# Optimization experiments

Measured on AMD Instinct MI355X. Metric: run time of the kernel, lower is better.

## Reference

```python
import jax, jax.numpy as jnp
import numpy as np

NUM_NODES = 50000
NUM_EDGES = 800000
NUM_GRAPHS = 64
EMBED = 128
HIDDEN = 128
LAYERS = 3
CLUSTERS = 16
OUT_DIM = 128
MAX_DEG = 64
EPS = 1e-5


def setup_inputs() -> dict:
    key = jax.random.key(0)
    ks = jax.random.split(key, 16)
    deg_idx = jax.random.randint(ks[0], (NUM_NODES,), 0, MAX_DEG + 1)
    edge_index = jax.random.randint(ks[1], (2, NUM_EDGES), 0, NUM_NODES)
    batch = jnp.sort(jax.random.randint(ks[2], (NUM_NODES,), 0, NUM_GRAPHS))
    s = 0.05
    emb = jax.random.normal(ks[3], (MAX_DEG + 1, EMBED), jnp.float32) * s
    Wl = jax.random.normal(ks[4], (LAYERS, HIDDEN, HIDDEN), jnp.float32) * s
    bl = jnp.zeros((LAYERS, HIDDEN), jnp.float32)
    Wr = jax.random.normal(ks[5], (LAYERS, HIDDEN, HIDDEN), jnp.float32) * s
    gamma = jnp.ones((LAYERS, HIDDEN), jnp.float32)
    beta = jnp.zeros((LAYERS, HIDDEN), jnp.float32)
    attn_W = jax.random.normal(ks[6], (HIDDEN, CLUSTERS), jnp.float32) * s
    attn_b = jnp.zeros((CLUSTERS,), jnp.float32)
    out_W = jax.random.normal(ks[7], (HIDDEN, OUT_DIM), jnp.float32) * s
    out_b = jnp.zeros((OUT_DIM,), jnp.float32)
    return {"emb": emb, "Wl": Wl, "bl": bl, "Wr": Wr, "gamma": gamma,
            "beta": beta, "attn_W": attn_W, "attn_b": attn_b,
            "out_W": out_W, "out_b": out_b, "deg_idx": deg_idx,
            "edge_index": edge_index, "batch": batch}


def reference(emb, Wl, bl, Wr, gamma, beta, attn_W, attn_b, out_W, out_b,
              deg_idx, edge_index, batch):
    N = deg_idx.shape[0]
    src, dst = edge_index[0], edge_index[1]
    x = emb[deg_idx]  # [N, EMBED]
    for l in range(Wl.shape[0]):
        # SAGEConv (mean aggr): lin_l(mean_j x_j) + lin_r(x); lin_r has no bias
        msg_sum = jax.ops.segment_sum(x[src], dst, num_segments=N)
        cnt = jax.ops.segment_sum(jnp.ones((src.shape[0], 1), x.dtype), dst,
                                  num_segments=N)
        mean = msg_sum / jnp.maximum(cnt, 1.0)
        x = mean @ Wl[l] + bl[l] + x @ Wr[l]
        # BatchNorm1d (training-mode batch stats, biased variance)
        mu = x.mean(axis=0)
        var = jnp.mean((x - mu) ** 2, axis=0)
        x = (x - mu) * jax.lax.rsqrt(var + EPS) * gamma[l] + beta[l]
        x = jax.nn.relu(x)  # dropout is identity in eval
    scores = x @ attn_W + attn_b  # [N, C] (num_heads == 1 -> squeeze)
    # per-graph softmax over nodes (segment softmax along dim 0)
    smax = jax.ops.segment_max(scores, batch, num_segments=NUM_GRAPHS)
    e = jnp.exp(scores - smax[batch])
    denom = jax.ops.segment_sum(e, batch, num_segments=NUM_GRAPHS)
    w = e / denom[batch]  # [N, C]
    # c_b = w_b^T @ x_b  -> segment-weighted sums: [B, C, H]
    clust = jax.ops.segment_sum(w[:, :, None] * x[:, None, :], batch,
                                num_segments=NUM_GRAPHS)
    return clust @ out_W + out_b  # [B, C, OUT_DIM]
```

## Files before the change

### kernel.cpp

```cpp
#include <hip/hip_runtime.h>

typedef unsigned short u16;
typedef unsigned int   u32;

#define H    128
#define C    16
#define ODIM 128

typedef short bf16x8 __attribute__((ext_vector_type(8)));
typedef float f32x4  __attribute__((ext_vector_type(4)));
typedef float f32x2v __attribute__((ext_vector_type(2)));

#define WSP 272
#define NP  256

__device__ __forceinline__ float bf2f(u32 v){
  union { u32 i; float f; } t; t.i = v << 16; return t.f;
}
__device__ __forceinline__ u16 f2bf(float f){
  u32 u = __float_as_uint(f);
  u32 r = u + 0x7fffu + ((u >> 16) & 1u);
  return (u16)(r >> 16);
}
__device__ __forceinline__ u32 pack2(float a, float b){
  return (u32)f2bf(a) | ((u32)f2bf(b) << 16);
}
__device__ __forceinline__ u32 pack_fp8x4(float a, float b, float c, float d){
  int p = __builtin_amdgcn_cvt_pk_fp8_f32(a, b, 0, false);
  p     = __builtin_amdgcn_cvt_pk_fp8_f32(c, d, p, true);
  return (u32)p;
}

__global__ __launch_bounds__(256) void k_setup(const float* __restrict__ emb,
    const int* __restrict__ deg, u16* __restrict__ xb, u32* __restrict__ xq,
    const int* __restrict__ batch, int* __restrict__ gs,
    const float* __restrict__ Wl, const float* __restrict__ Wr,
    u16* __restrict__ Wt, const int* __restrict__ ei,
    int* __restrict__ blkhist, int N, int B, int NB, int E, int chunk,
    int g0, int g1, int g2){
  __shared__ __align__(16) char smem[4608];
  int bid = blockIdx.x, tid = threadIdx.x;
  if (bid < g0){
    int i = bid*256 + tid;
    if (i < N*32){
      int n = i >> 5, q = i & 31;
      int d = deg[n];
      float4 v = ((const float4*)(emb + (size_t)d*H))[q];
      uint2 o; o.x = pack2(v.x, v.y); o.y = pack2(v.z, v.w);
      ((uint2*)(xb + (size_t)n*H))[q] = o;
      xq[i] = pack_fp8x4(v.x, v.y, v.z, v.w);
    }
  } else if (bid < g1){
    int n = (bid - g0)*256 + tid;
    if (n < N){
      int b = batch[n];
      if (n == 0){ for (int g = 0; g <= b; g++) gs[g] = 0; }
      else {
        int pb = batch[n-1];
        for (int g = pb+1; g <= b; g++) gs[g] = n;
      }
      if (n == N-1){ for (int g = b+1; g <= B; g++) gs[g] = N; }
    }
  } else if (bid < g2){
    u16 (*T)[18] = (u16(*)[18])smem;
    int b = bid - g1;
    int strip = b & 7, half = (b >> 3) & 1, l = b >> 4;
    const float* M = (half ? Wr : Wl) + (size_t)l*H*H;
    int k0 = strip * 16;
    #pragma unroll
    for (int j = 0; j < 8; j++){
      int u = tid + j*256;
      int kk = u >> 7, h = u & 127;
      T[h][kk] = f2bf(M[(size_t)(k0 + kk)*H + h]);
    }
    __syncthreads();
    #pragma unroll
    for (int j = 0; j < 8; j++){
      int u = tid + j*256;
      int h = u >> 4, k16 = u & 15;
      Wt[((size_t)(l*H + h))*256 + half*128 + k0 + k16] = T[h][k16];
    }
  } else {
    int* hist = (int*)smem;
    int blk = bid - g2;
    for (int b = tid; b < NB; b += 256) hist[b] = 0;
    __syncthreads();
    int start = blk*chunk, end = min(E, start + chunk);
    for (int e = start + tid; e < end; e += 256)
      atomicAdd(&hist[ei[E + e] >> 7], 1);
    __syncthreads();
    for (int b = tid; b < NB; b += 256) blkhist[b*NP + blk] = hist[b];
  }
}

__global__ __launch_bounds__(256) void k_scanA(const int* __restrict__ in,
    int* __restrict__ out, int* __restrict__ bsum, int n){
  __shared__ int wsum[4];
  int tid = threadIdx.x;
  int base = blockIdx.x*1024 + tid*4;
  int v0 = (base+0 < n) ? in[base+0] : 0;
  int v1 = (base+1 < n) ? in[base+1] : 0;
  int v2 = (base+2 < n) ? in[base+2] : 0;
  int v3 = (base+3 < n) ? in[base+3] : 0;
  int tsum = v0+v1+v2+v3;
  int lane = tid & 63, w = tid >> 6;
  int incl = tsum;
  for (int d = 1; d < 64; d <<= 1){
    int t = __shfl_up(incl, d, 64);
    if (lane >= d) incl += t;
  }
  if (lane == 63) wsum[w] = incl;
  __syncthreads();
  int woff = 0;
  for (int i = 0; i < w; i++) woff += wsum[i];
  int excl = woff + incl - tsum;
  if (base+0 < n) out[base+0] = excl;
  if (base+1 < n) out[base+1] = excl + v0;
  if (base+2 < n) out[base+2] = excl + v0 + v1;
  if (base+3 < n) out[base+3] = excl + v0 + v1 + v2;
  if (tid == 255) bsum[blockIdx.x] = woff + incl;
}

__global__ __launch_bounds__(256) void k_scanB(const int* __restrict__ bsum,
    int* __restrict__ boff, int nb){
  __shared__ int ws[4];
  int tid = threadIdx.x;
  int v = (tid < nb) ? bsum[tid] : 0;
  int lane = tid & 63, w = tid >> 6;
  int incl = v;
  for (int d = 1; d < 64; d <<= 1){
    int t = __shfl_up(incl, d, 64);
    if (lane >= d) incl += t;
  }
  if (lane == 63) ws[w] = incl;
  __syncthreads();
  int woff = 0;
  for (int i = 0; i < w; i++) woff += ws[i];
  boff[tid] = woff + incl - v;
}

__global__ __launch_bounds__(256) void k_scanC(int* __restrict__ out,
    const int* __restrict__ boff, int n){
  int i = blockIdx.x*256 + threadIdx.x;
  if (i < n) out[i] += boff[i >> 10];
}

__global__ __launch_bounds__(256) void k_place(const int* __restrict__ ei,
    const int* __restrict__ bases, int2* __restrict__ pairs,
    int NB, int E, int chunk){
  __shared__ int cursor[400];
  int blk = blockIdx.x, tid = threadIdx.x;
  for (int b = tid; b < NB; b += 256) cursor[b] = bases[b*NP + blk];
  __syncthreads();
  int start = blk*chunk, end = min(E, start + chunk);
  for (int e = start + tid; e < end; e += 256){
    int s = ei[e], d = ei[E + e];
    int pos = atomicAdd(&cursor[d >> 7], 1);
    pairs[pos] = make_int2(s, d);
  }
}

__global__ __launch_bounds__(256) void k_cnt_place(const int2* __restrict__ pairs,
    const int* __restrict__ bases, int* __restrict__ rowptr,
    int* __restrict__ col, int NB, int N, int E){
  int b = blockIdx.x, tid = threadIdx.x;
  int bstart = bases[b*NP];
  int bend   = (b+1 < NB) ? bases[(b+1)*NP] : E;
  __shared__ int cnt[128], sc[128], rank[128];
  if (tid < 128) cnt[tid] = 0;
  __syncthreads();
  for (int e = bstart + tid; e < bend; e += 256)
    atomicAdd(&cnt[pairs[e].y & 127], 1);
  __syncthreads();
  if (tid < 128) sc[tid] = cnt[tid];
  for (int d = 1; d < 128; d <<= 1){
    int v = 0;
    __syncthreads();
    if (tid < 128 && tid >= d) v = sc[tid - d];
    __syncthreads();
    if (tid < 128) sc[tid] += v;
  }
  __syncthreads();
  if (tid < 128){
    int excl = sc[tid] - cnt[tid];
    rank[tid] = bstart + excl;
    int node = b*128 + tid;
    if (node < N) rowptr[node] = bstart + excl;
  }
  if (b == NB-1 && tid == 0) rowptr[N] = E;
  __syncthreads();
  for (int e = bstart + tid; e < bend; e += 256){
    int2 p = pairs[e];
    int pos = atomicAdd(&rank[p.y & 127], 1);
    col[pos] = p.x;
  }
}

__global__ __launch_bounds__(256) void k_agg(const u32* __restrict__ xq,
    const int* __restrict__ rowptr, const int* __restrict__ col,
    u16* __restrict__ meanb, int N){
  int wid  = (blockIdx.x*256 + threadIdx.x) >> 6;
  int lane = threadIdx.x & 63;
  if (wid >= N) return;
  int r0 = rowptr[wid], r1 = rowptr[wid+1];
  int grp = lane >> 4, fl = lane & 15;
  const u32* xf = xq + fl*2;
  float a0=0.f,a1=0.f,a2=0.f,a3=0.f,a4=0.f,a5=0.f,a6=0.f,a7=0.f;
  int e = r0 + grp;
  for (; e + 4 < r1; e += 8){
    uint2 v = *(const uint2*)(xf + (size_t)col[e]*32);
    uint2 u = *(const uint2*)(xf + (size_t)col[e+4]*32);
    f32x2v p0 = __builtin_amdgcn_cvt_pk_f32_fp8((int)v.x, false);
    f32x2v p1 = __builtin_amdgcn_cvt_pk_f32_fp8((int)v.x, true);
    f32x2v p2 = __builtin_amdgcn_cvt_pk_f32_fp8((int)v.y, false);
    f32x2v p3 = __builtin_amdgcn_cvt_pk_f32_fp8((int)v.y, true);
    f32x2v q0 = __builtin_amdgcn_cvt_pk_f32_fp8((int)u.x, false);
    f32x2v q1 = __builtin_amdgcn_cvt_pk_f32_fp8((int)u.x, true);
    f32x2v q2 = __builtin_amdgcn_cvt_pk_f32_fp8((int)u.y, false);
    f32x2v q3 = __builtin_amdgcn_cvt_pk_f32_fp8((int)u.y, true);
    a0 += p0.x + q0.x; a1 += p0.y + q0.y;
    a2 += p1.x + q1.x; a3 += p1.y + q1.y;
    a4 += p2.x + q2.x; a5 += p2.y + q2.y;
    a6 += p3.x + q3.x; a7 += p3.y + q3.y;
  }
  if (e < r1){
    uint2 v = *(const uint2*)(xf + (size_t)col[e]*32);
    f32x2v p0 = __builtin_amdgcn_cvt_pk_f32_fp8((int)v.x, false);
    f32x2v p1 = __builtin_amdgcn_cvt_pk_f32_fp8((int)v.x, true);
    f32x2v p2 = __builtin_amdgcn_cvt_pk_f32_fp8((int)v.y, false);
    f32x2v p3 = __builtin_amdgcn_cvt_pk_f32_fp8((int)v.y, true);
    a0 += p0.x; a1 += p0.y; a2 += p1.x; a3 += p1.y;
    a4 += p2.x; a5 += p2.y; a6 += p3.x; a7 += p3.y;
  }
  a0 += __shfl_xor(a0,16,64); a1 += __shfl_xor(a1,16,64);
  a2 += __shfl_xor(a2,16,64); a3 += __shfl_xor(a3,16,64);
  a4 += __shfl_xor(a4,16,64); a5 += __shfl_xor(a5,16,64);
  a6 += __shfl_xor(a6,16,64); a7 += __shfl_xor(a7,16,64);
  a0 += __shfl_xor(a0,32,64); a1 += __shfl_xor(a1,32,64);
  a2 += __shfl_xor(a2,32,64); a3 += __shfl_xor(a3,32,64);
  a4 += __shfl_xor(a4,32,64); a5 += __shfl_xor(a5,32,64);
  a6 += __shfl_xor(a6,32,64); a7 += __shfl_xor(a7,32,64);
  if (grp == 0){
    float invc = 1.0f / (float)max(r1 - r0, 1);
    uint4 o;
    o.x = pack2(a0*invc, a1*invc);
    o.y = pack2(a2*invc, a3*invc);
    o.z = pack2(a4*invc, a5*invc);
    o.w = pack2(a6*invc, a7*invc);
    *(uint4*)(meanb + (size_t)wid*H + fl*8) = o;
  }
}

__global__ __launch_bounds__(256) void k_linear(const u16* __restrict__ meanb,
    const u16* __restrict__ xb, const u16* __restrict__ Wt,
    const float* __restrict__ bl, float* __restrict__ x2,
    float* __restrict__ pstats, int N){
  __shared__ u16 Ws[128][WSP];
  __shared__ float Sh[128], Qh[128];
  int tid = threadIdx.x;
  if (tid < 128){ Sh[tid] = 0.f; Qh[tid] = 0.f; }
  int lane = tid & 63, w = tid >> 6;
  int mlane = lane & 15, quad = lane >> 4;
  int node = blockIdx.x*64 + w*16 + mlane;
  const u16* arow_m = meanb + (size_t)node*H + quad*8;
  const u16* arow_x = xb   + (size_t)node*H + quad*8;
  bf16x8 af[8];
  #pragma unroll
  for (int kk = 0; kk < 4; kk++){
    af[kk]     = *(const bf16x8*)(arow_m + kk*32);
    af[kk + 4] = *(const bf16x8*)(arow_x + kk*32);
  }
  #pragma unroll
  for (int j = 0; j < 16; j++){
    int u = tid + j*256;
    int row = u >> 5, seg = u & 31;
    uint4 v = ((const uint4*)(Wt + (size_t)row*256))[seg];
    *(uint4*)&Ws[row][seg*8] = v;
  }
  __syncthreads();
  f32x4 acc[8];
  #pragma unroll
  for (int t = 0; t < 8; t++) acc[t] = (f32x4){0.f, 0.f, 0.f, 0.f};
  #pragma unroll
  for (int kk = 0; kk < 8; kk++){
    #pragma unroll
    for (int t = 0; t < 8; t++){
      bf16x8 b = *(const bf16x8*)&Ws[t*16 + mlane][kk*32 + quad*8];
      acc[t] = __builtin_amdgcn_mfma_f32_16x16x32_bf16(af[kk], b, acc[t], 0, 0, 0);
    }
  }
  #pragma unroll
  for (int t = 0; t < 8; t++){
    int h = t*16 + mlane;
    float bv = bl[h];
    float s = 0.f, q = 0.f;
    #pragma unroll
    for (int r = 0; r < 4; r++){
      int nd = blockIdx.x*64 + w*16 + quad*4 + r;
      if (nd < N){
        float v = acc[t][r] + bv;
        x2[(size_t)nd*H + h] = v;
        s += v; q = fmaf(v, v, q);
      }
    }
    s += __shfl_xor(s, 16, 64); s += __shfl_xor(s, 32, 64);
    q += __shfl_xor(q, 16, 64); q += __shfl_xor(q, 32, 64);
    if (quad == 0){
      atomicAdd(&Sh[h], s);
      atomicAdd(&Qh[h], q);
    }
  }
  __syncthreads();
  {
    float v = (tid < 128) ? Sh[tid] : Qh[tid - 128];
    pstats[(size_t)blockIdx.x*256 + tid] = v;
  }
}

__global__ __launch_bounds__(256) void k_statred(const float* __restrict__ pstats,
    float* __restrict__ stats, int nblk){
  __shared__ float red[4];
  int c = blockIdx.x, tid = threadIdx.x;
  float s = 0.f;
  for (int b = tid; b < nblk; b += 256)
    s += pstats[(size_t)b*256 + c];
  s += __shfl_xor(s, 1, 64);  s += __shfl_xor(s, 2, 64);
  s += __shfl_xor(s, 4, 64);  s += __shfl_xor(s, 8, 64);
  s += __shfl_xor(s, 16, 64); s += __shfl_xor(s, 32, 64);
  if ((tid & 63) == 0) red[tid >> 6] = s;
  __syncthreads();
  if (tid == 0) stats[c] = red[0] + red[1] + red[2] + red[3];
}

__global__ __launch_bounds__(256) void k_bnrelu(const float* __restrict__ x2,
    const float* __restrict__ stats, const float* __restrict__ gamma,
    const float* __restrict__ beta, u16* __restrict__ xb, u32* __restrict__ xq,
    int N, float invN,
    const float* __restrict__ attn_W, const float* __restrict__ attn_b,
    float* __restrict__ escore, int do_scores){
  __shared__ float xs[8][132];
  __shared__ float aw[H*C];
  __shared__ float ab[C];
  int tid = threadIdx.x;
  int i = blockIdx.x*256 + tid;
  bool active = (i < N*32);
  int h = (tid & 31) * 4;
  float r[4] = {0.f, 0.f, 0.f, 0.f};
  if (active){
    float4 v = ((const float4*)x2)[i];
    float vv[4] = {v.x, v.y, v.z, v.w};
    #pragma unroll
    for (int j = 0; j < 4; j++){
      float mu  = stats[h+j] * invN;
      float var = fmaf(-mu, mu, stats[H + h + j] * invN);
      float sc  = rsqrtf(var + 1e-5f) * gamma[h+j];
      float bi  = beta[h+j];
      r[j] = fmaxf(fmaf(vv[j] - mu, sc, bi), 0.0f);
    }
    uint2 o; o.x = pack2(r[0], r[1]); o.y = pack2(r[2], r[3]);
    ((uint2*)xb)[i] = o;
    xq[i] = pack_fp8x4(r[0], r[1], r[2], r[3]);
  }
  if (do_scores){
    #pragma unroll
    for (int j = 0; j < 8; j++) aw[tid + j*256] = attn_W[tid + j*256];
    if (tid < C) ab[tid] = attn_b[tid];
    int ln = tid >> 5;
    if (active){
      xs[ln][h+0]=r[0]; xs[ln][h+1]=r[1]; xs[ln][h+2]=r[2]; xs[ln][h+3]=r[3];
    }
    __syncthreads();
    if (tid < 128){
      int n2 = tid >> 4, c = tid & 15;
      int node = blockIdx.x*8 + n2;
      if (node < N){
        float acc = ab[c];
        #pragma unroll 4
        for (int k = 0; k < H; k++)
          acc = fmaf(xs[n2][k], aw[k*C + c], acc);
        escore[(size_t)node*C + c] = __expf(acc);
      }
    }
  }
}

__global__ __launch_bounds__(256) void k_denom(const float* __restrict__ escore,
    const int* __restrict__ gs, float* __restrict__ gsum){
  int g = blockIdx.x;
  int c = threadIdx.x & 15, sub = threadIdx.x >> 4;
  int a = gs[g], b = gs[g+1];
  float s = 0.f;
  for (int n = a + sub; n < b; n += 16) s += escore[(size_t)n*C + c];
  __shared__ float part[16][17];
  part[sub][c] = s;
  for (int off2 = 8; off2 > 0; off2 >>= 1){
    __syncthreads();
    if (sub < off2) part[sub][c] += part[sub + off2][c];
  }
  __syncthreads();
  if (threadIdx.x < C) gsum[(size_t)g*C + threadIdx.x] = part[0][threadIdx.x];
}

__global__ __launch_bounds__(256) void k_clust(const u16* __restrict__ xb,
    const float* __restrict__ escore, const int* __restrict__ gs,
    float* __restrict__ partial){
  int g = blockIdx.x >> 4, b = blockIdx.x & 15;
  int h = threadIdx.x & 127, cg = threadIdx.x >> 7;
  int a = gs[g], e2 = gs[g+1];
  float acc[8] = {0,0,0,0,0,0,0,0};
  for (int n = a + b; n < e2; n += 16){
    float xv = bf2f(xb[(size_t)n*H + h]);
    const float4* ep = (const float4*)(escore + (size_t)n*C) + cg*2;
    float4 e0 = ep[0], e1 = ep[1];
    acc[0] = fmaf(e0.x, xv, acc[0]);
    acc[1] = fmaf(e0.y, xv, acc[1]);
    acc[2] = fmaf(e0.z, xv, acc[2]);
    acc[3] = fmaf(e0.w, xv, acc[3]);
    acc[4] = fmaf(e1.x, xv, acc[4]);
    acc[5] = fmaf(e1.y, xv, acc[5]);
    acc[6] = fmaf(e1.z, xv, acc[6]);
    acc[7] = fmaf(e1.w, xv, acc[7]);
  }
  int c0 = cg*8;
  float* dst = partial + (((size_t)(g*16 + b))*C)*H + h;
  #pragma unroll
  for (int r = 0; r < 8; r++)
    dst[(size_t)(c0 + r)*H] = acc[r];
}

__global__ __launch_bounds__(256) void k_out(const float* __restrict__ partial,
    const float* __restrict__ gsum, const float* __restrict__ out_W,
    const float* __restrict__ out_b, float* __restrict__ out){
  __shared__ float cs[2][128];
  int tid = threadIdx.x;
  int r = tid >> 7, h = tid & 127;
  int row = blockIdx.x*2 + r;
  int g = row >> 4, c = row & 15;
  float s = 0.f;
  for (int b = 0; b < 16; b++)
    s += partial[(((size_t)(g*16 + b))*C + c)*H + h];
  cs[r][h] = s;
  __syncthreads();
  float gden = gsum[row];
  float inv = gden > 0.f ? 1.0f / gden : 0.f;
  float acc = 0.f;
  for (int hh = 0; hh < H; hh++)
    acc = fmaf(cs[r][hh], out_W[hh*ODIM + h], acc);
  out[(size_t)row*ODIM + h] = fmaf(acc, inv, out_b[h]);
}

extern "C" void kernel_launch(void* const* d_in, const int* in_sizes, int n_in,
                              void* d_out, int out_size, void* d_ws, size_t ws_size,
                              hipStream_t stream){
  const float* emb    = (const float*)d_in[0];
  const float* Wl     = (const float*)d_in[1];
  const float* bl     = (const float*)d_in[2];
  const float* Wr     = (const float*)d_in[3];
  const float* gamma  = (const float*)d_in[4];
  const float* beta   = (const float*)d_in[5];
  const float* attn_W = (const float*)d_in[6];
  const float* attn_b = (const float*)d_in[7];
  const float* out_W  = (const float*)d_in[8];
  const float* out_b  = (const float*)d_in[9];
  const int* deg    = (const int*)d_in[10];
  const int* ei     = (const int*)d_in[11];
  const int* batch  = (const int*)d_in[12];
  float* out = (float*)d_out;

  const int N = in_sizes[10];
  const int E = in_sizes[11] / 2;
  const int L = in_sizes[1] / (H*H);
  const int B = out_size / (C*ODIM);
  const int NB = (N + 127) >> 7;
  const int nbh = NB * NP;
  const int chunk = (E + NP - 1) / NP;
  const int nblkL = (N + 63) / 64;

  size_t off = 0;
  auto alloc = [&](size_t bytes) -> void* {
    void* p = (char*)d_ws + off;
    off += (bytes + 255) & ~(size_t)255;
    return p;
  };
  u16*   xb     = (u16*)  alloc((size_t)N*H*2);
  u32*   xq     = (u32*)  alloc((size_t)N*H);
  u16*   meanb  = (u16*)  alloc((size_t)N*H*2);
  float* x2     = (float*)alloc((size_t)N*H*4);
  int2*  pairs  = (int2*)x2;
  float* partial= x2;
  u16*   Wt     = (u16*)  alloc((size_t)L*H*256*2);
  float* escore = (float*)alloc((size_t)N*C*4);
  int*   col    = (int*)  alloc((size_t)E*4);
  int*   rowptr = (int*)  alloc((size_t)(N+1)*4);
  int*   blkhist= (int*)  alloc((size_t)nbh*4);
  int*   bases  = (int*)  alloc((size_t)nbh*4);
  int*   bsum   = (int*)  alloc(256*4);
  int*   boff   = (int*)  alloc(256*4);
  int*   gs     = (int*)  alloc((size_t)(B+1)*4);
  float* gsum   = (float*)alloc((size_t)B*C*4);
  float* stats  = (float*)alloc((size_t)L*2*H*4);
  float* pstats = (float*)alloc((size_t)nblkL*256*4);

  int g0 = (N*32 + 255)/256;
  int g1 = g0 + (N + 255)/256;
  int g2 = g1 + L*16;
  int gT = g2 + NP;
  hipLaunchKernelGGL(k_setup, dim3(gT), dim3(256), 0, stream,
                     emb, deg, xb, xq, batch, gs, Wl, Wr, Wt, ei, blkhist,
                     N, B, NB, E, chunk, g0, g1, g2);
  int nblkS = (nbh + 1023) / 1024;
  hipLaunchKernelGGL(k_scanA,  dim3(nblkS), dim3(256), 0, stream, blkhist, bases, bsum, nbh);
  hipLaunchKernelGGL(k_scanB,  dim3(1),     dim3(256), 0, stream, bsum, boff, nblkS);
  hipLaunchKernelGGL(k_scanC,  dim3((nbh+255)/256), dim3(256), 0, stream, bases, boff, nbh);
  hipLaunchKernelGGL(k_place,  dim3(NP), dim3(256), 0, stream, ei, bases, pairs, NB, E, chunk);
  hipLaunchKernelGGL(k_cnt_place, dim3(NB), dim3(256), 0, stream, pairs, bases, rowptr, col, NB, N, E);

  float invN = 1.0f / (float)N;
  for (int l = 0; l < L; l++){
    hipLaunchKernelGGL(k_agg,    dim3((N+3)/4),  dim3(256), 0, stream, xq, rowptr, col, meanb, N);
    hipLaunchKernelGGL(k_linear, dim3(nblkL),    dim3(256), 0, stream,
                       meanb, xb, Wt + (size_t)l*H*256, bl + (size_t)l*H, x2,
                       pstats, N);
    hipLaunchKernelGGL(k_statred,dim3(256),      dim3(256), 0, stream, pstats, stats + l*2*H, nblkL);
    hipLaunchKernelGGL(k_bnrelu, dim3((N*32+255)/256), dim3(256), 0, stream,
                       x2, stats + l*2*H, gamma + (size_t)l*H, beta + (size_t)l*H,
                       xb, xq, N, invN, attn_W, attn_b, escore, (l == L-1) ? 1 : 0);
  }
  hipLaunchKernelGGL(k_denom,  dim3(B),     dim3(256), 0, stream, escore, gs, gsum);
  hipLaunchKernelGGL(k_clust,  dim3(B*16),  dim3(256), 0, stream, xb, escore, gs, partial);
  hipLaunchKernelGGL(k_out,    dim3(B*C/2), dim3(256), 0, stream, partial, gsum, out_W, out_b, out);
}
```

Before: 337.5 us.

## Fold scan offsets into placement, widen fp8 gather loads, fuse softmax denominator into output

Removes the k_scanC pass by adding the block offset when the bases are read in k_place and k_cnt_place. Changes k_agg so 8 lanes each read 16 fp8 features (uint4) per neighbour, covering 8 edges per step instead of 4, which means wider loads and more edges in flight. Drops k_denom: k_out now sums the per-graph softmax denominators itself with wave shuffles. Two launches go away, but k_out rereads escore once per output row pair, and the extra shuffle stage in k_agg raises register pressure.

```diff
diff --git a/kernel.cpp b/kernel.cpp
--- a/kernel.cpp
+++ b/kernel.cpp
@@ -139,18 +139,15 @@
   boff[tid] = woff + incl - v;
 }
 
-__global__ __launch_bounds__(256) void k_scanC(int* __restrict__ out,
-    const int* __restrict__ boff, int n){
-  int i = blockIdx.x*256 + threadIdx.x;
-  if (i < n) out[i] += boff[i >> 10];
-}
-
 __global__ __launch_bounds__(256) void k_place(const int* __restrict__ ei,
-    const int* __restrict__ bases, int2* __restrict__ pairs,
-    int NB, int E, int chunk){
+    const int* __restrict__ bases, const int* __restrict__ boff,
+    int2* __restrict__ pairs, int NB, int E, int chunk){
   __shared__ int cursor[400];
   int blk = blockIdx.x, tid = threadIdx.x;
-  for (int b = tid; b < NB; b += 256) cursor[b] = bases[b*NP + blk];
+  for (int b = tid; b < NB; b += 256){
+    int i = b*NP + blk;
+    cursor[b] = bases[i] + boff[i >> 10];
+  }
   __syncthreads();
   int start = blk*chunk, end = min(E, start + chunk);
   for (int e = start + tid; e < end; e += 256){
@@ -161,11 +158,13 @@
 }
 
 __global__ __launch_bounds__(256) void k_cnt_place(const int2* __restrict__ pairs,
-    const int* __restrict__ bases, int* __restrict__ rowptr,
-    int* __restrict__ col, int NB, int N, int E){
+    const int* __restrict__ bases, const int* __restrict__ boff,
+    int* __restrict__ rowptr, int* __restrict__ col, int NB, int N, int E){
   int b = blockIdx.x, tid = threadIdx.x;
-  int bstart = bases[b*NP];
-  int bend   = (b+1 < NB) ? bases[(b+1)*NP] : E;
+  int i0 = b*NP;
+  int bstart = bases[i0] + boff[i0 >> 10];
+  int bend = E;
+  if (b+1 < NB){ int i1 = (b+1)*NP; bend = bases[i1] + boff[i1 >> 10]; }
   __shared__ int cnt[128], sc[128], rank[128];
   if (tid < 128) cnt[tid] = 0;
   __syncthreads();
@@ -196,6 +195,18 @@
   }
 }
 
+__device__ __forceinline__ void dec16(float* a, uint4 v){
+  f32x2v p;
+  p = __builtin_amdgcn_cvt_pk_f32_fp8((int)v.x, false); a[0]+=p.x; a[1]+=p.y;
+  p = __builtin_amdgcn_cvt_pk_f32_fp8((int)v.x, true ); a[2]+=p.x; a[3]+=p.y;
+  p = __builtin_amdgcn_cvt_pk_f32_fp8((int)v.y, false); a[4]+=p.x; a[5]+=p.y;
+  p = __builtin_amdgcn_cvt_pk_f32_fp8((int)v.y, true ); a[6]+=p.x; a[7]+=p.y;
+  p = __builtin_amdgcn_cvt_pk_f32_fp8((int)v.z, false); a[8]+=p.x; a[9]+=p.y;
+  p = __builtin_amdgcn_cvt_pk_f32_fp8((int)v.z, true ); a[10]+=p.x; a[11]+=p.y;
+  p = __builtin_amdgcn_cvt_pk_f32_fp8((int)v.w, false); a[12]+=p.x; a[13]+=p.y;
+  p = __builtin_amdgcn_cvt_pk_f32_fp8((int)v.w, true ); a[14]+=p.x; a[15]+=p.y;
+}
+
 __global__ __launch_bounds__(256) void k_agg(const u32* __restrict__ xq,
     const int* __restrict__ rowptr, const int* __restrict__ col,
     u16* __restrict__ meanb, int N){
@@ -203,51 +214,42 @@
   int lane = threadIdx.x & 63;
   if (wid >= N) return;
   int r0 = rowptr[wid], r1 = rowptr[wid+1];
-  int grp = lane >> 4, fl = lane & 15;
-  const u32* xf = xq + fl*2;
-  float a0=0.f,a1=0.f,a2=0.f,a3=0.f,a4=0.f,a5=0.f,a6=0.f,a7=0.f;
+  int grp = lane >> 3, fl = lane & 7;
+  const u32* xf = xq + fl*4;
+  float a[16];
+  #pragma unroll
+  for (int j = 0; j < 16; j++) a[j] = 0.f;
   int e = r0 + grp;
-  for (; e + 4 < r1; e += 8){
-    uint2 v = *(const uint2*)(xf + (size_t)col[e]*32);
-    uint2 u = *(const uint2*)(xf + (size_t)col[e+4]*32);
-    f32x2v p0 = __builtin_amdgcn_cvt_pk_f32_fp8((int)v.x, false);
-    f32x2v p1 = __builtin_amdgcn_cvt_pk_f32_fp8((int)v.x, true);
-    f32x2v p2 = __builtin_amdgcn_cvt_pk_f32_fp8((int)v.y, false);
-    f32x2v p3 = __builtin_amdgcn_cvt_pk_f32_fp8((int)v.y, true);
-    f32x2v q0 = __builtin_amdgcn_cvt_pk_f32_fp8((int)u.x, false);
-    f32x2v q1 = __builtin_amdgcn_cvt_pk_f32_fp8((int)u.x, true);
-    f32x2v q2 = __builtin_amdgcn_cvt_pk_f32_fp8((int)u.y, false);
-    f32x2v q3 = __builtin_amdgcn_cvt_pk_f32_fp8((int)u.y, true);
-    a0 += p0.x + q0.x; a1 += p0.y + q0.y;
-    a2 += p1.x + q1.x; a3 += p1.y + q1.y;
-    a4 += p2.x + q2.x; a5 += p2.y + q2.y;
-    a6 += p3.x + q3.x; a7 += p3.y + q3.y;
+  for (; e + 8 < r1; e += 16){
+    uint4 v = *(const uint4*)(xf + (size_t)col[e]*32);
+    uint4 u = *(const uint4*)(xf + (size_t)col[e+8]*32);
+    dec16(a, v);
+    dec16(a, u);
   }
   if (e < r1){
-    uint2 v = *(const uint2*)(xf + (size_t)col[e]*32);
-    f32x2v p0 = __builtin_amdgcn_cvt_pk_f32_fp8((int)v.x, false);
-    f32x2v p1 = __builtin_amdgcn_cvt_pk_f32_fp8((int)v.x, true);
-    f32x2v p2 = __builtin_amdgcn_cvt_pk_f32_fp8((int)v.y, false);
-    f32x2v p3 = __builtin_amdgcn_cvt_pk_f32_fp8((int)v.y, true);
-    a0 += p0.x; a1 += p0.y; a2 += p1.x; a3 += p1.y;
-    a4 += p2.x; a5 += p2.y; a6 += p3.x; a7 += p3.y;
-  }
-  a0 += __shfl_xor(a0,16,64); a1 += __shfl_xor(a1,16,64);
-  a2 += __shfl_xor(a2,16,64); a3 += __shfl_xor(a3,16,64);
-  a4 += __shfl_xor(a4,16,64); a5 += __shfl_xor(a5,16,64);
-  a6 += __shfl_xor(a6,16,64); a7 += __shfl_xor(a7,16,64);
-  a0 += __shfl_xor(a0,32,64); a1 += __shfl_xor(a1,32,64);
-  a2 += __shfl_xor(a2,32,64); a3 += __shfl_xor(a3,32,64);
-  a4 += __shfl_xor(a4,32,64); a5 += __shfl_xor(a5,32,64);
-  a6 += __shfl_xor(a6,32,64); a7 += __shfl_xor(a7,32,64);
+    uint4 v = *(const uint4*)(xf + (size_t)col[e]*32);
+    dec16(a, v);
+  }
+  #pragma unroll
+  for (int j = 0; j < 16; j++){
+    a[j] += __shfl_xor(a[j], 8, 64);
+    a[j] += __shfl_xor(a[j], 16, 64);
+    a[j] += __shfl_xor(a[j], 32, 64);
+  }
   if (grp == 0){
     float invc = 1.0f / (float)max(r1 - r0, 1);
-    uint4 o;
-    o.x = pack2(a0*invc, a1*invc);
-    o.y = pack2(a2*invc, a3*invc);
-    o.z = pack2(a4*invc, a5*invc);
-    o.w = pack2(a6*invc, a7*invc);
-    *(uint4*)(meanb + (size_t)wid*H + fl*8) = o;
+    uint4 o0, o1;
+    o0.x = pack2(a[0]*invc,  a[1]*invc);
+    o0.y = pack2(a[2]*invc,  a[3]*invc);
+    o0.z = pack2(a[4]*invc,  a[5]*invc);
+    o0.w = pack2(a[6]*invc,  a[7]*invc);
+    o1.x = pack2(a[8]*invc,  a[9]*invc);
+    o1.y = pack2(a[10]*invc, a[11]*invc);
+    o1.z = pack2(a[12]*invc, a[13]*invc);
+    o1.w = pack2(a[14]*invc, a[15]*invc);
+    u16* mp = meanb + (size_t)wid*H + fl*16;
+    *(uint4*)mp       = o0;
+    *(uint4*)(mp + 8) = o1;
   }
 }
 
@@ -384,23 +386,6 @@
   }
 }
 
-__global__ __launch_bounds__(256) void k_denom(const float* __restrict__ escore,
-    const int* __restrict__ gs, float* __restrict__ gsum){
-  int g = blockIdx.x;
-  int c = threadIdx.x & 15, sub = threadIdx.x >> 4;
-  int a = gs[g], b = gs[g+1];
-  float s = 0.f;
-  for (int n = a + sub; n < b; n += 16) s += escore[(size_t)n*C + c];
-  __shared__ float part[16][17];
-  part[sub][c] = s;
-  for (int off2 = 8; off2 > 0; off2 >>= 1){
-    __syncthreads();
-    if (sub < off2) part[sub][c] += part[sub + off2][c];
-  }
-  __syncthreads();
-  if (threadIdx.x < C) gsum[(size_t)g*C + threadIdx.x] = part[0][threadIdx.x];
-}
-
 __global__ __launch_bounds__(256) void k_clust(const u16* __restrict__ xb,
     const float* __restrict__ escore, const int* __restrict__ gs,
     float* __restrict__ partial){
@@ -429,19 +414,28 @@
 }
 
 __global__ __launch_bounds__(256) void k_out(const float* __restrict__ partial,
-    const float* __restrict__ gsum, const float* __restrict__ out_W,
-    const float* __restrict__ out_b, float* __restrict__ out){
+    const float* __restrict__ escore, const int* __restrict__ gs,
+    const float* __restrict__ out_W, const float* __restrict__ out_b,
+    float* __restrict__ out){
   __shared__ float cs[2][128];
+  __shared__ float dsum[4];
   int tid = threadIdx.x;
   int r = tid >> 7, h = tid & 127;
   int row = blockIdx.x*2 + r;
   int g = row >> 4, c = row & 15;
+  int a = gs[g], b2 = gs[g+1];
   float s = 0.f;
+  for (int n = a + h; n < b2; n += 128) s += escore[(size_t)n*C + c];
+  s += __shfl_xor(s, 1, 64);  s += __shfl_xor(s, 2, 64);
+  s += __shfl_xor(s, 4, 64);  s += __shfl_xor(s, 8, 64);
+  s += __shfl_xor(s, 16, 64); s += __shfl_xor(s, 32, 64);
+  if ((tid & 63) == 0) dsum[tid >> 6] = s;
+  float p = 0.f;
   for (int b = 0; b < 16; b++)
-    s += partial[(((size_t)(g*16 + b))*C + c)*H + h];
-  cs[r][h] = s;
-  __syncthreads();
-  float gden = gsum[row];
+    p += partial[(((size_t)(g*16 + b))*C + c)*H + h];
+  cs[r][h] = p;
+  __syncthreads();
+  float gden = dsum[r*2] + dsum[r*2 + 1];
   float inv = gden > 0.f ? 1.0f / gden : 0.f;
   float acc = 0.f;
   for (int hh = 0; hh < H; hh++)
@@ -497,7 +491,6 @@
   int*   bsum   = (int*)  alloc(256*4);
   int*   boff   = (int*)  alloc(256*4);
   int*   gs     = (int*)  alloc((size_t)(B+1)*4);
-  float* gsum   = (float*)alloc((size_t)B*C*4);
   float* stats  = (float*)alloc((size_t)L*2*H*4);
   float* pstats = (float*)alloc((size_t)nblkL*256*4);
 
@@ -511,9 +504,8 @@
   int nblkS = (nbh + 1023) / 1024;
   hipLaunchKernelGGL(k_scanA,  dim3(nblkS), dim3(256), 0, stream, blkhist, bases, bsum, nbh);
   hipLaunchKernelGGL(k_scanB,  dim3(1),     dim3(256), 0, stream, bsum, boff, nblkS);
-  hipLaunchKernelGGL(k_scanC,  dim3((nbh+255)/256), dim3(256), 0, stream, bases, boff, nbh);
-  hipLaunchKernelGGL(k_place,  dim3(NP), dim3(256), 0, stream, ei, bases, pairs, NB, E, chunk);
-  hipLaunchKernelGGL(k_cnt_place, dim3(NB), dim3(256), 0, stream, pairs, bases, rowptr, col, NB, N, E);
+  hipLaunchKernelGGL(k_place,  dim3(NP), dim3(256), 0, stream, ei, bases, boff, pairs, NB, E, chunk);
+  hipLaunchKernelGGL(k_cnt_place, dim3(NB), dim3(256), 0, stream, pairs, bases, boff, rowptr, col, NB, N, E);
 
   float invN = 1.0f / (float)N;
   for (int l = 0; l < L; l++){
@@ -526,7 +518,6 @@
                        x2, stats + l*2*H, gamma + (size_t)l*H, beta + (size_t)l*H,
                        xb, xq, N, invN, attn_W, attn_b, escore, (l == L-1) ? 1 : 0);
   }
-  hipLaunchKernelGGL(k_denom,  dim3(B),     dim3(256), 0, stream, escore, gs, gsum);
   hipLaunchKernelGGL(k_clust,  dim3(B*16),  dim3(256), 0, stream, xb, escore, gs, partial);
-  hipLaunchKernelGGL(k_out,    dim3(B*C/2), dim3(256), 0, stream, partial, gsum, out_W, out_b, out);
-}
+  hipLaunchKernelGGL(k_out,    dim3(B*C/2), dim3(256), 0, stream, partial, escore, gs, out_W, out_b, out);
+}
```

New measurement: 334.0 us. Within noise of the previous version (-1.0%).
